# Kernel tuning notes

Measured on AMD Instinct MI355X. Metric: run time of the kernel, lower is better.

The kernel has to match this reference:

```python
import jax, jax.numpy as jnp
import numpy as np

V, E, HID, NLAYERS, NL, B, T = 21128, 512, 512, 2, 9, 64, 512
H = HID // 2  # per-direction hidden


def setup_inputs() -> dict:
    key = jax.random.key(0)
    ks = jax.random.split(key, 12)
    n = lambda k, sh, sc=0.05: (jax.random.normal(k, sh, dtype=jnp.float32) * sc)
    return {
        "input_ids": jax.random.randint(ks[0], (B, T), 0, V),
        "labels": jax.random.randint(ks[1], (B, T), 0, NL),
        "emb": n(ks[2], (V, E), 0.02),
        # stacked LSTM params: [layer, direction, ...]; layer0 input = E == HID
        "w_ih": n(ks[3], (NLAYERS, 2, 4 * H, HID)),
        "w_hh": n(ks[4], (NLAYERS, 2, 4 * H, H)),
        "b_ih": n(ks[5], (NLAYERS, 2, 4 * H)),
        "b_hh": n(ks[6], (NLAYERS, 2, 4 * H)),
        "cls_w": n(ks[7], (NL, HID)),
        "cls_b": n(ks[8], (NL,)),
        "start_trans": jax.random.uniform(ks[9], (NL,), jnp.float32, -0.1, 0.1),
        "end_trans": jax.random.uniform(ks[10], (NL,), jnp.float32, -0.1, 0.1),
        "trans": jax.random.uniform(ks[11], (NL, NL), jnp.float32, -0.1, 0.1),
    }


def _lstm_dir(x, wi, wh, bi, bh, reverse):
    # x: [B,T,I] -> h: [B,T,H]; torch gate order i,f,g,o
    xp = jnp.einsum('bti,gi->btg', x, wi) + bi + bh  # [B,T,4H]
    if reverse:
        xp = xp[:, ::-1]
    h0 = jnp.zeros((x.shape[0], wh.shape[1]), x.dtype)

    def step(carry, xt):
        h, c = carry
        g = xt + h @ wh.T
        i, f, gg, o = jnp.split(g, 4, axis=-1)
        c = jax.nn.sigmoid(f) * c + jax.nn.sigmoid(i) * jnp.tanh(gg)
        h = jax.nn.sigmoid(o) * jnp.tanh(c)
        return (h, c), h

    _, hs = jax.lax.scan(step, (h0, h0), xp.swapaxes(0, 1))
    hs = hs.swapaxes(0, 1)
    return hs[:, ::-1] if reverse else hs


def _crf_neg_llh(logits, labels, start_trans, end_trans, trans):
    # torchcrf forward, full mask, reduction='sum'; returns -sum(log-likelihood)
    em0 = logits[:, 0]  # [B,NL]
    alpha0 = start_trans[None, :] + em0
    num0 = start_trans[labels[:, 0]] + jnp.take_along_axis(em0, labels[:, 0:1], 1)[:, 0]

    def step(carry, xt):
        alpha, num, prev = carry
        em, tag = xt  # [B,NL], [B]
        alpha = jax.nn.logsumexp(alpha[:, :, None] + trans[None] + em[:, None, :], axis=1)
        num = num + trans[prev, tag] + jnp.take_along_axis(em, tag[:, None], 1)[:, 0]
        return (alpha, num, tag), None

    xs = (logits[:, 1:].swapaxes(0, 1), labels[:, 1:].swapaxes(0, 1))
    (alpha, num, last), _ = jax.lax.scan(step, (alpha0, num0, labels[:, 0]), xs)
    denom = jax.nn.logsumexp(alpha + end_trans[None, :], axis=1)
    num = num + end_trans[last]
    return -jnp.sum(num - denom)


def reference(input_ids, labels, emb, w_ih, w_hh, b_ih, b_hh, cls_w, cls_b,
              start_trans, end_trans, trans):
    x = emb[input_ids]  # [B,T,E]
    for l in range(NLAYERS):
        fwd = _lstm_dir(x, w_ih[l, 0], w_hh[l, 0], b_ih[l, 0], b_hh[l, 0], False)
        bwd = _lstm_dir(x, w_ih[l, 1], w_hh[l, 1], b_ih[l, 1], b_hh[l, 1], True)
        x = jnp.concatenate([fwd, bwd], axis=-1)  # [B,T,HID]
    logits = jnp.einsum('bth,lh->btl', x, cls_w) + cls_b  # [B,T,NL]
    return _crf_neg_llh(logits, labels, start_trans, end_trans, trans)
```

## Files before the change

kernel.cpp:

```cpp
#include <hip/hip_runtime.h>

#define B_   64
#define T_   512
#define HID_ 512
#define H_   256
#define G4   1024
#define N2   2048
#define M_   (B_*T_)
#define NL_  9

typedef short short8 __attribute__((ext_vector_type(8)));
typedef float f32x4 __attribute__((ext_vector_type(4)));
typedef _Float16 f16x2 __attribute__((ext_vector_type(2)));

__device__ inline float bf2f(unsigned short u) {
  unsigned int x = ((unsigned int)u) << 16;
  return __builtin_bit_cast(float, x);
}
__device__ inline unsigned short f2bf(float f) {
  unsigned int u = __builtin_bit_cast(unsigned int, f);
  return (unsigned short)((u + 0x7fffu + ((u >> 16) & 1u)) >> 16);
}
__device__ inline unsigned short f2h(float f) {
  _Float16 h = (_Float16)f;
  return __builtin_bit_cast(unsigned short, h);
}
__device__ inline float fdot2(unsigned int w, unsigned int h, float acc) {
#if __has_builtin(__builtin_amdgcn_fdot2)
  return __builtin_amdgcn_fdot2(__builtin_bit_cast(f16x2, w),
                                __builtin_bit_cast(f16x2, h), acc, false);
#else
  f16x2 a = __builtin_bit_cast(f16x2, w), b = __builtin_bit_cast(f16x2, h);
  return acc + (float)a[0]*(float)b[0] + (float)a[1]*(float)b[1];
#endif
}
__device__ inline float sigm(float x)     { return 1.f / (1.f + __expf(-x)); }
__device__ inline float tanhfast(float x) { return 1.f - 2.f / (__expf(2.f*x) + 1.f); }

__device__ inline float xhalf_sum(float x) {
#if __has_builtin(__builtin_amdgcn_permlane32_swap)
  typedef unsigned int u32x2 __attribute__((ext_vector_type(2)));
  u32x2 r = __builtin_amdgcn_permlane32_swap(
      __builtin_bit_cast(unsigned int, x), __builtin_bit_cast(unsigned int, x),
      false, false);
  return x + __builtin_bit_cast(float, r[1]);
#else
  return x + __shfl_xor(x, 32, 64);
#endif
}

__device__ inline void gload16(const unsigned short* g, unsigned short* l) {
  __builtin_amdgcn_global_load_lds(
      (const __attribute__((address_space(1))) void*)g,
      (__attribute__((address_space(3))) void*)l, 16, 0, 0);
}

__global__ void k_cast_bf16x4(const float4* __restrict__ src, ushort4* __restrict__ dst, int n4) {
  int i = blockIdx.x*256 + threadIdx.x;
  if (i < n4) {
    float4 v = src[i];
    ushort4 o;
    o.x = f2bf(v.x); o.y = f2bf(v.y); o.z = f2bf(v.z); o.w = f2bf(v.w);
    dst[i] = o;
  }
}

__global__ void k_pack_whh(const float* __restrict__ whh, unsigned int* __restrict__ wr,
                           unsigned int* __restrict__ wl) {
  int idx = blockIdx.x*256 + threadIdx.x;
  int q   = idx & 3;
  int t   = (idx >> 2) & 511;
  int i4  = (idx >> 11) & 63;
  int ld  = idx >> 17;
  int lane = t & 63, wave = t >> 6;
  int u  = wave*32 + (lane & 31);
  int kh = lane >> 5;
  int g, k0;
  if (i4 < 48) { g = i4/12; int j = i4%12; k0 = kh*128 + 8*j + 2*q; }
  else         { int m = i4-48; g = m>>2; int jl = m&3; k0 = kh*128 + 96 + 8*jl + 2*q; }
  int c = g*256 + u;
  const float* src = whh + ((size_t)ld*1024 + c)*256 + k0;
  unsigned int pack = (unsigned int)f2h(src[0]) | ((unsigned int)f2h(src[1]) << 16);
  if (i4 < 48) wr[(((size_t)ld*48 + i4)*512 + t)*4 + q] = pack;
  else         wl[(((size_t)ld*16 + (i4-48))*512 + t)*4 + q] = pack;
}

__global__ void k_bias_sum(const float* __restrict__ bi, const float* __restrict__ bh,
                           float* __restrict__ bs) {
  int i = blockIdx.x*256 + threadIdx.x;
  if (i < 4096) {
    int l = i >> 11, r = i & 2047;
    int dd = r >> 10, nn = r & 1023, g = nn >> 8, u = nn & 255;
    bs[l*2048 + dd*1024 + u*4 + g] = bi[i] + bh[i];
  }
}

__global__ void k_cls_pad(const float* __restrict__ w, unsigned short* __restrict__ dst) {
  int i = blockIdx.x*256 + threadIdx.x;
  if (i < 16*512) {
    int n = i >> 9, k = i & 511;
    dst[i] = (n < NL_) ? f2bf(w[n*512 + k]) : (unsigned short)0;
  }
}

__global__ void k_embed(const int* __restrict__ ids, const float* __restrict__ emb,
                        unsigned short* __restrict__ x0) {
  int idx = blockIdx.x*256 + threadIdx.x;
  int m  = idx >> 7;
  int e4 = (idx & 127) << 2;
  int id = ids[m];
  float4 v = *(const float4*)(emb + (size_t)id*HID_ + e4);
  ushort4 o;
  o.x = f2bf(v.x); o.y = f2bf(v.y); o.z = f2bf(v.z); o.w = f2bf(v.w);
  *(ushort4*)(x0 + (size_t)m*HID_ + e4) = o;
}

__global__ __launch_bounds__(256) void k_gemm_inproj(const unsigned short* __restrict__ A,
    const unsigned short* __restrict__ Bt, const float* __restrict__ bias,
    unsigned short* __restrict__ C) {
  __shared__ unsigned short As[2][4096];
  __shared__ unsigned short Bs[2][4096];
  int tid  = threadIdx.x;
  int lane = tid & 63, w = tid >> 6;
  int wm = w >> 1, wn = w & 1;
  int d  = blockIdx.x >> 3;
  int u0 = (blockIdx.x & 7) * 32;
  int m0 = blockIdx.y * 128;

  int c0 = tid, c1 = 256 + tid;
  int ar0 = c0 & 127, ak0 = c0 >> 7;
  int ar1 = c1 & 127, ak1 = c1 >> 7;
  int br0 = d*1024 + (ar0 >> 5)*256 + u0 + (ar0 & 31);
  int br1 = d*1024 + (ar1 >> 5)*256 + u0 + (ar1 & 31);
  const unsigned short* gA0 = A  + (size_t)(m0 + ar0)*512 + ak0*8;
  const unsigned short* gA1 = A  + (size_t)(m0 + ar1)*512 + ak1*8;
  const unsigned short* gB0 = Bt + (size_t)br0*512 + ak0*8;
  const unsigned short* gB1 = Bt + (size_t)br1*512 + ak1*8;

  int r = lane & 15, kg = lane >> 4;

  f32x4 acc[4][4];
  #pragma unroll
  for (int mi = 0; mi < 4; mi++)
    #pragma unroll
    for (int ni = 0; ni < 4; ni++)
      acc[mi][ni] = (f32x4){0,0,0,0};

  gload16(gA0, As[0] + c0*8); gload16(gA1, As[0] + c1*8);
  gload16(gB0, Bs[0] + c0*8); gload16(gB1, Bs[0] + c1*8);
  gA0 += 32; gA1 += 32; gB0 += 32; gB1 += 32;
  __syncthreads();

  int cur = 0;
  #pragma unroll 1
  for (int kt = 0; kt < 16; kt++) {
    if (kt < 15) {
      unsigned short* nA = As[cur^1];
      unsigned short* nB = Bs[cur^1];
      gload16(gA0, nA + c0*8); gload16(gA1, nA + c1*8);
      gload16(gB0, nB + c0*8); gload16(gB1, nB + c1*8);
      gA0 += 32; gA1 += 32; gB0 += 32; gB1 += 32;
    }
    const short8* Af = (const short8*)As[cur] + (size_t)kg*128 + wm*64 + r;
    const short8* Bf = (const short8*)Bs[cur] + (size_t)kg*128 + wn*16 + r;
    short8 av[4], bv[4];
    #pragma unroll
    for (int i = 0; i < 4; i++) { av[i] = Af[i*16]; bv[i] = Bf[i*32]; }
    #pragma unroll
    for (int mi = 0; mi < 4; mi++)
      #pragma unroll
      for (int ni = 0; ni < 4; ni++)
        acc[mi][ni] = __builtin_amdgcn_mfma_f32_16x16x32_bf16(av[mi], bv[ni], acc[mi][ni], 0, 0, 0);
    __syncthreads();
    cur ^= 1;
  }

  int rbase = m0 + wm*64 + (lane >> 4)*4;
  int ucol  = u0 + wn*16 + (lane & 15);
  float4 bb = *(const float4*)(bias + (size_t)d*1024 + ucol*4);
  #pragma unroll
  for (int mi = 0; mi < 4; mi++)
    #pragma unroll
    for (int rr = 0; rr < 4; rr++) {
      ushort4 o;
      o.x = f2bf(acc[mi][0][rr] + bb.x);
      o.y = f2bf(acc[mi][1][rr] + bb.y);
      o.z = f2bf(acc[mi][2][rr] + bb.z);
      o.w = f2bf(acc[mi][3][rr] + bb.w);
      *(ushort4*)(C + (size_t)(rbase + mi*16 + rr)*N2 + d*1024 + ucol*4) = o;
    }
}

__global__ __launch_bounds__(256) void k_cls(const unsigned short* __restrict__ X,
    const unsigned short* __restrict__ Wb, const float* __restrict__ cb,
    float* __restrict__ out) {
  int lane = threadIdx.x & 63, wave = threadIdx.x >> 6;
  int m0 = blockIdx.x*64 + wave*16;
  int r = lane & 15, kg = lane >> 4;
  const short8* Ap = (const short8*)(X  + (size_t)(m0 + r)*512 + kg*8);
  const short8* Bp = (const short8*)(Wb + (size_t)r*512 + kg*8);
  f32x4 acc = {0,0,0,0};
  #pragma unroll
  for (int kb = 0; kb < 16; kb++)
    acc = __builtin_amdgcn_mfma_f32_16x16x32_bf16(Ap[kb*4], Bp[kb*4], acc, 0, 0, 0);
  int row0 = m0 + (lane >> 4)*4, col = lane & 15;
  if (col < NL_) {
    float bb = cb[col];
    #pragma unroll
    for (int rr = 0; rr < 4; rr++)
      out[(size_t)(row0+rr)*NL_ + col] = acc[rr] + bb;
  }
}

#define DOT4(ACC, W0, W1, W2, W3, HH) do { \
  ACC = fdot2(W0, (HH).x, ACC); ACC = fdot2(W1, (HH).y, ACC); \
  ACC = fdot2(W2, (HH).z, ACC); ACC = fdot2(W3, (HH).w, ACC); } while(0)

__global__ __launch_bounds__(512, 2) void k_rec(const unsigned short* __restrict__ xp,
    const uint4* __restrict__ wr, const uint4* __restrict__ wl,
    unsigned short* __restrict__ xout, int layer) {
  extern __shared__ char smem[];
  unsigned int* hA = (unsigned int*)(smem + 131072);
  unsigned int* hB = hA + 128;
  int t = threadIdx.x;
  int lane = t & 63, wave = t >> 6;
  int u  = wave*32 + (lane & 31);
  int kh = lane >> 5;
  bool lo = (lane < 32);
  int b = blockIdx.x >> 1, d = blockIdx.x & 1;
  int ld = layer*2 + d;

  char* wlb = smem + (((unsigned)(t*16)) ^ (((unsigned)t & 0x38u) << 1));
  {
    const uint4* src = wl + (size_t)ld*16*512 + t;
    #pragma unroll
    for (int m = 0; m < 16; m++)
      *(uint4*)(wlb + m*8192) = src[(size_t)m*512];
  }
  uint4 wq[48];
  {
    const uint4* src = wr + (size_t)ld*48*512 + t;
    #pragma unroll
    for (int i = 0; i < 48; i++) wq[i] = src[(size_t)i*512];
  }
  if (t < 128) hA[t] = 0u;
  float cst = 0.f;
  const unsigned short* xbase = xp + (size_t)b*T_*N2 + (size_t)d*G4 + u*4;
  unsigned short* obase = xout + (size_t)b*T_*HID_ + d*H_ + u;
  __syncthreads();

  int tt = d ? (T_-1) : 0;
  ushort4 nx = *(const ushort4*)(xbase + (size_t)tt*N2);
  #pragma unroll 1
  for (int step = 0; step < T_; step++) {
    int ttn = d ? (T_-2-step) : (step+1);
    int ttc = (step < T_-1) ? ttn : tt;
    ushort4 cx = nx;
    nx = *(const ushort4*)(xbase + (size_t)ttc*N2);
    const uint4* hs = (const uint4*)((step & 1) ? hB : hA) + kh*16;
    float a0 = lo ? bf2f(cx.x) : 0.f;
    float a1 = lo ? bf2f(cx.y) : 0.f;
    float a2 = lo ? bf2f(cx.z) : 0.f;
    float a3 = lo ? bf2f(cx.w) : 0.f;
    #pragma unroll
    for (int j = 0; j < 12; j++) {
      uint4 hh = hs[j];
      DOT4(a0, wq[j].x,    wq[j].y,    wq[j].z,    wq[j].w,    hh);
      DOT4(a1, wq[12+j].x, wq[12+j].y, wq[12+j].z, wq[12+j].w, hh);
      DOT4(a2, wq[24+j].x, wq[24+j].y, wq[24+j].z, wq[24+j].w, hh);
      DOT4(a3, wq[36+j].x, wq[36+j].y, wq[36+j].z, wq[36+j].w, hh);
    }
    #pragma unroll
    for (int jl = 0; jl < 4; jl++) {
      uint4 hh = hs[12 + jl];
      uint4 q0 = *(const uint4*)(wlb + (0*4+jl)*8192);
      uint4 q1 = *(const uint4*)(wlb + (1*4+jl)*8192);
      uint4 q2 = *(const uint4*)(wlb + (2*4+jl)*8192);
      uint4 q3 = *(const uint4*)(wlb + (3*4+jl)*8192);
      DOT4(a0, q0.x, q0.y, q0.z, q0.w, hh);
      DOT4(a1, q1.x, q1.y, q1.z, q1.w, hh);
      DOT4(a2, q2.x, q2.y, q2.z, q2.w, hh);
      DOT4(a3, q3.x, q3.y, q3.z, q3.w, hh);
    }
    a0 = xhalf_sum(a0); a1 = xhalf_sum(a1);
    a2 = xhalf_sum(a2); a3 = xhalf_sum(a3);
    if (lo) {
      float gi = sigm(a0);
      float gf = sigm(a1);
      float gg = tanhfast(a2);
      float go = sigm(a3);
      cst = gf*cst + gi*gg;
      float h = go * tanhfast(cst);
      _Float16* hn = (_Float16*)((step & 1) ? hA : hB);
      hn[u] = (_Float16)h;
      obase[(size_t)tt*HID_] = f2bf(h);
    }
    asm volatile("s_waitcnt lgkmcnt(0)" ::: "memory");
    __builtin_amdgcn_s_barrier();
    tt = ttn;
  }
}

__global__ void k_zero(float* out) { if (threadIdx.x == 0) out[0] = 0.f; }

__global__ void k_crf(const float* __restrict__ logits, const int* __restrict__ labels,
                      const float* __restrict__ st, const float* __restrict__ et,
                      const float* __restrict__ tr, float* __restrict__ out) {
  int b = blockIdx.x, lane = threadIdx.x;
  bool act = lane < NL_;
  const float* lb = logits + (size_t)b*T_*NL_;
  float trc[9];
  #pragma unroll
  for (int i = 0; i < 9; i++) trc[i] = act ? tr[i*9 + lane] : 0.f;
  float em = act ? lb[lane] : -1e30f;
  float alpha = act ? (st[lane] + em) : -1e30f;
  int prev = labels[b*T_];
  float num = __shfl(alpha, prev);
  for (int ttt = 1; ttt < T_; ttt++) {
    em = act ? lb[ttt*NL_ + lane] : -1e30f;
    float vv[9]; float mx = -1e30f;
    #pragma unroll
    for (int i = 0; i < 9; i++) { vv[i] = __shfl(alpha, i) + trc[i]; mx = fmaxf(mx, vv[i]); }
    float s = 0.f;
    #pragma unroll
    for (int i = 0; i < 9; i++) s += __expf(vv[i] - mx);
    alpha = act ? (mx + __logf(s) + em) : -1e30f;
    int tag = labels[b*T_ + ttt];
    float emtag = __shfl(em, tag);
    if (lane == 0) num += tr[prev*9 + tag] + emtag;
    prev = tag;
  }
  float fa = act ? (alpha + et[lane]) : -1e30f;
  float mx = -1e30f;
  #pragma unroll
  for (int i = 0; i < 9; i++) mx = fmaxf(mx, __shfl(fa, i));
  float s = 0.f;
  #pragma unroll
  for (int i = 0; i < 9; i++) s += __expf(__shfl(fa, i) - mx);
  float denom = mx + __logf(s);
  if (lane == 0) {
    num += et[prev];
    atomicAdd(out, denom - num);
  }
}

extern "C" void kernel_launch(void* const* d_in, const int* in_sizes, int n_in,
                              void* d_out, int out_size, void* d_ws, size_t ws_size,
                              hipStream_t stream) {
  const int*   ids    = (const int*)d_in[0];
  const int*   labels = (const int*)d_in[1];
  const float* emb    = (const float*)d_in[2];
  const float* w_ih   = (const float*)d_in[3];
  const float* w_hh   = (const float*)d_in[4];
  const float* b_ih   = (const float*)d_in[5];
  const float* b_hh   = (const float*)d_in[6];
  const float* cls_w  = (const float*)d_in[7];
  const float* cls_b  = (const float*)d_in[8];
  const float* st     = (const float*)d_in[9];
  const float* et     = (const float*)d_in[10];
  const float* tr     = (const float*)d_in[11];
  float* out = (float*)d_out;

  char* ws = (char*)d_ws;
  unsigned short* xp    = (unsigned short*)(ws);
  unsigned short* x0    = (unsigned short*)(ws + 134217728);
  unsigned short* x1    = (unsigned short*)(ws + 167772160);
  unsigned short* wbi   = (unsigned short*)(ws + 201326592);
  unsigned int*   wreg  = (unsigned int*)  (ws + 205520896);
  unsigned int*   wldsg = (unsigned int*)  (ws + 207093760);
  float*          bsum  = (float*)         (ws + 207618048);
  unsigned short* clswb = (unsigned short*)(ws + 207634432);
  float*          logit = (float*)         (ws + 207650816);

  const int REC_SMEM = 131072 + 1024;
  hipFuncSetAttribute((const void*)k_rec, hipFuncAttributeMaxDynamicSharedMemorySize, REC_SMEM);

  k_cast_bf16x4<<<2048, 256, 0, stream>>>((const float4*)w_ih, (ushort4*)wbi, 2*N2*512/4);
  k_pack_whh <<<2048, 256, 0, stream>>>(w_hh, wreg, wldsg);
  k_bias_sum <<<16,   256, 0, stream>>>(b_ih, b_hh, bsum);
  k_cls_pad  <<<32,   256, 0, stream>>>(cls_w, clswb);
  k_embed    <<<16384,256, 0, stream>>>(ids, emb, x0);

  dim3 ggrid(16, 256);
  k_gemm_inproj<<<ggrid, 256, 0, stream>>>(x0, wbi, bsum, xp);
  k_rec<<<128, 512, REC_SMEM, stream>>>(xp, (const uint4*)wreg, (const uint4*)wldsg, x1, 0);
  k_gemm_inproj<<<ggrid, 256, 0, stream>>>(x1, wbi + (size_t)N2*512, bsum + 2048, xp);
  k_rec<<<128, 512, REC_SMEM, stream>>>(xp, (const uint4*)wreg, (const uint4*)wldsg, x0, 1);
  k_cls<<<512, 256, 0, stream>>>(x0, clswb, cls_b, logit);
  k_zero<<<1, 64, 0, stream>>>(out);
  k_crf<<<64, 64, 0, stream>>>(logit, labels, st, et, tr, out);
}
```

Before: 2.358 ms.

## Split recurrent hidden reduction four ways with two units per lane group

The recurrent LSTM kernel now splits the 256-wide hidden dot product into four 64-element quarters across lane groups of 16, and each lane group handles two hidden units (eight gate accumulators) instead of one unit split into halves. The weight packing is reorganized to match, the h buffer is padded per quarter to avoid LDS bank conflicts, and partial sums are combined with permlane32 and permlane16 swaps. The goal is more useful work per lane, so the gate nonlinearities run on a quarter of the lanes instead of half and the cross-lane reduction is shared. In exchange there is an extra reduction stage per gate and more accumulator registers.

New measurement: 2.925 ms. 24.0% more time.

```diff
diff --git a/kernel.cpp b/kernel.cpp
--- a/kernel.cpp
+++ b/kernel.cpp
@@ -12,6 +12,7 @@
 typedef short short8 __attribute__((ext_vector_type(8)));
 typedef float f32x4 __attribute__((ext_vector_type(4)));
 typedef _Float16 f16x2 __attribute__((ext_vector_type(2)));
+typedef unsigned int u32x2 __attribute__((ext_vector_type(2)));
 
 __device__ inline float bf2f(unsigned short u) {
   unsigned int x = ((unsigned int)u) << 16;
@@ -37,16 +38,24 @@
 __device__ inline float sigm(float x)     { return 1.f / (1.f + __expf(-x)); }
 __device__ inline float tanhfast(float x) { return 1.f - 2.f / (__expf(2.f*x) + 1.f); }
 
-__device__ inline float xhalf_sum(float x) {
+__device__ inline float qsum(float x) {
 #if __has_builtin(__builtin_amdgcn_permlane32_swap)
-  typedef unsigned int u32x2 __attribute__((ext_vector_type(2)));
   u32x2 r = __builtin_amdgcn_permlane32_swap(
       __builtin_bit_cast(unsigned int, x), __builtin_bit_cast(unsigned int, x),
       false, false);
-  return x + __builtin_bit_cast(float, r[1]);
+  x += __builtin_bit_cast(float, r[1]);
 #else
-  return x + __shfl_xor(x, 32, 64);
+  x += __shfl_xor(x, 32, 64);
 #endif
+#if __has_builtin(__builtin_amdgcn_permlane16_swap)
+  u32x2 s = __builtin_amdgcn_permlane16_swap(
+      __builtin_bit_cast(unsigned int, x), __builtin_bit_cast(unsigned int, x),
+      false, false);
+  x += __builtin_bit_cast(float, s[1]);
+#else
+  x += __shfl_xor(x, 16, 64);
+#endif
+  return x;
 }
 
 __device__ inline void gload16(const unsigned short* g, unsigned short* l) {
@@ -68,21 +77,23 @@
 __global__ void k_pack_whh(const float* __restrict__ whh, unsigned int* __restrict__ wr,
                            unsigned int* __restrict__ wl) {
   int idx = blockIdx.x*256 + threadIdx.x;
-  int q   = idx & 3;
+  int qq  = idx & 3;
   int t   = (idx >> 2) & 511;
   int i4  = (idx >> 11) & 63;
   int ld  = idx >> 17;
   int lane = t & 63, wave = t >> 6;
-  int u  = wave*32 + (lane & 31);
-  int kh = lane >> 5;
-  int g, k0;
-  if (i4 < 48) { g = i4/12; int j = i4%12; k0 = kh*128 + 8*j + 2*q; }
-  else         { int m = i4-48; g = m>>2; int jl = m&3; k0 = kh*128 + 96 + 8*jl + 2*q; }
-  int c = g*256 + u;
-  const float* src = whh + ((size_t)ld*1024 + c)*256 + k0;
+  int q = lane >> 4, p = lane & 15;
+  int P = wave*16 + p;
+  int c, j;
+  if (i4 < 48) { c = i4/6; j = i4%6; }
+  else         { int m = i4-48; c = m>>1; j = 6 + (m&1); }
+  int unit_sel = c >> 2, g = c & 3;
+  int col = g*256 + 2*P + unit_sel;
+  int k0  = q*64 + 8*j + 2*qq;
+  const float* src = whh + ((size_t)ld*1024 + col)*256 + k0;
   unsigned int pack = (unsigned int)f2h(src[0]) | ((unsigned int)f2h(src[1]) << 16);
-  if (i4 < 48) wr[(((size_t)ld*48 + i4)*512 + t)*4 + q] = pack;
-  else         wl[(((size_t)ld*16 + (i4-48))*512 + t)*4 + q] = pack;
+  if (i4 < 48) wr[(((size_t)ld*48 + i4)*512 + t)*4 + qq] = pack;
+  else         wl[(((size_t)ld*16 + (i4-48))*512 + t)*4 + qq] = pack;
 }
 
 __global__ void k_bias_sum(const float* __restrict__ bi, const float* __restrict__ bh,
@@ -220,13 +231,12 @@
     const uint4* __restrict__ wr, const uint4* __restrict__ wl,
     unsigned short* __restrict__ xout, int layer) {
   extern __shared__ char smem[];
-  unsigned int* hA = (unsigned int*)(smem + 131072);
-  unsigned int* hB = hA + 128;
+  char* hAb = smem + 131072;
+  char* hBb = hAb + 576;
   int t = threadIdx.x;
   int lane = t & 63, wave = t >> 6;
-  int u  = wave*32 + (lane & 31);
-  int kh = lane >> 5;
-  bool lo = (lane < 32);
+  int q = lane >> 4, p = lane & 15;
+  int P = wave*16 + p;
   int b = blockIdx.x >> 1, d = blockIdx.x & 1;
   int ld = layer*2 + d;
 
@@ -243,57 +253,76 @@
     #pragma unroll
     for (int i = 0; i < 48; i++) wq[i] = src[(size_t)i*512];
   }
-  if (t < 128) hA[t] = 0u;
-  float cst = 0.f;
-  const unsigned short* xbase = xp + (size_t)b*T_*N2 + (size_t)d*G4 + u*4;
-  unsigned short* obase = xout + (size_t)b*T_*HID_ + d*H_ + u;
+  if (t < 144) ((unsigned int*)hAb)[t] = 0u;
+  float cst0 = 0.f, cst1 = 0.f;
+  const unsigned short* xbase = xp + (size_t)b*T_*N2 + (size_t)d*G4 + P*8;
+  unsigned short* obase = xout + (size_t)b*T_*HID_ + d*H_ + 2*P;
+  int hwoff = ((2*P) >> 6)*144 + ((2*P) & 63)*2;
   __syncthreads();
 
   int tt = d ? (T_-1) : 0;
-  ushort4 nx = *(const ushort4*)(xbase + (size_t)tt*N2);
+  uint4 nx = *(const uint4*)(xbase + (size_t)tt*N2);
   #pragma unroll 1
   for (int step = 0; step < T_; step++) {
     int ttn = d ? (T_-2-step) : (step+1);
     int ttc = (step < T_-1) ? ttn : tt;
-    ushort4 cx = nx;
-    nx = *(const ushort4*)(xbase + (size_t)ttc*N2);
-    const uint4* hs = (const uint4*)((step & 1) ? hB : hA) + kh*16;
-    float a0 = lo ? bf2f(cx.x) : 0.f;
-    float a1 = lo ? bf2f(cx.y) : 0.f;
-    float a2 = lo ? bf2f(cx.z) : 0.f;
-    float a3 = lo ? bf2f(cx.w) : 0.f;
-    #pragma unroll
-    for (int j = 0; j < 12; j++) {
-      uint4 hh = hs[j];
+    uint4 cx = nx;
+    nx = *(const uint4*)(xbase + (size_t)ttc*N2);
+    const char* hb = ((step & 1) ? hBb : hAb) + q*144;
+    float a0=0.f,a1=0.f,a2=0.f,a3=0.f,a4=0.f,a5=0.f,a6=0.f,a7=0.f;
+    #pragma unroll
+    for (int j = 0; j < 6; j++) {
+      uint4 hh = *(const uint4*)(hb + j*16);
       DOT4(a0, wq[j].x,    wq[j].y,    wq[j].z,    wq[j].w,    hh);
-      DOT4(a1, wq[12+j].x, wq[12+j].y, wq[12+j].z, wq[12+j].w, hh);
-      DOT4(a2, wq[24+j].x, wq[24+j].y, wq[24+j].z, wq[24+j].w, hh);
-      DOT4(a3, wq[36+j].x, wq[36+j].y, wq[36+j].z, wq[36+j].w, hh);
+      DOT4(a1, wq[6+j].x,  wq[6+j].y,  wq[6+j].z,  wq[6+j].w,  hh);
+      DOT4(a2, wq[12+j].x, wq[12+j].y, wq[12+j].z, wq[12+j].w, hh);
+      DOT4(a3, wq[18+j].x, wq[18+j].y, wq[18+j].z, wq[18+j].w, hh);
+      DOT4(a4, wq[24+j].x, wq[24+j].y, wq[24+j].z, wq[24+j].w, hh);
+      DOT4(a5, wq[30+j].x, wq[30+j].y, wq[30+j].z, wq[30+j].w, hh);
+      DOT4(a6, wq[36+j].x, wq[36+j].y, wq[36+j].z, wq[36+j].w, hh);
+      DOT4(a7, wq[42+j].x, wq[42+j].y, wq[42+j].z, wq[42+j].w, hh);
     }
     #pragma unroll
-    for (int jl = 0; jl < 4; jl++) {
-      uint4 hh = hs[12 + jl];
-      uint4 q0 = *(const uint4*)(wlb + (0*4+jl)*8192);
-      uint4 q1 = *(const uint4*)(wlb + (1*4+jl)*8192);
-      uint4 q2 = *(const uint4*)(wlb + (2*4+jl)*8192);
-      uint4 q3 = *(const uint4*)(wlb + (3*4+jl)*8192);
+    for (int jj = 0; jj < 2; jj++) {
+      uint4 hh = *(const uint4*)(hb + (6+jj)*16);
+      uint4 q0 = *(const uint4*)(wlb + (0*2+jj)*8192);
+      uint4 q1 = *(const uint4*)(wlb + (1*2+jj)*8192);
+      uint4 q2 = *(const uint4*)(wlb + (2*2+jj)*8192);
+      uint4 q3 = *(const uint4*)(wlb + (3*2+jj)*8192);
+      uint4 q4 = *(const uint4*)(wlb + (4*2+jj)*8192);
+      uint4 q5 = *(const uint4*)(wlb + (5*2+jj)*8192);
+      uint4 q6 = *(const uint4*)(wlb + (6*2+jj)*8192);
+      uint4 q7 = *(const uint4*)(wlb + (7*2+jj)*8192);
       DOT4(a0, q0.x, q0.y, q0.z, q0.w, hh);
       DOT4(a1, q1.x, q1.y, q1.z, q1.w, hh);
       DOT4(a2, q2.x, q2.y, q2.z, q2.w, hh);
       DOT4(a3, q3.x, q3.y, q3.z, q3.w, hh);
+      DOT4(a4, q4.x, q4.y, q4.z, q4.w, hh);
+      DOT4(a5, q5.x, q5.y, q5.z, q5.w, hh);
+      DOT4(a6, q6.x, q6.y, q6.z, q6.w, hh);
+      DOT4(a7, q7.x, q7.y, q7.z, q7.w, hh);
     }
-    a0 = xhalf_sum(a0); a1 = xhalf_sum(a1);
-    a2 = xhalf_sum(a2); a3 = xhalf_sum(a3);
-    if (lo) {
-      float gi = sigm(a0);
-      float gf = sigm(a1);
-      float gg = tanhfast(a2);
-      float go = sigm(a3);
-      cst = gf*cst + gi*gg;
-      float h = go * tanhfast(cst);
-      _Float16* hn = (_Float16*)((step & 1) ? hA : hB);
-      hn[u] = (_Float16)h;
-      obase[(size_t)tt*HID_] = f2bf(h);
+    a0 = qsum(a0); a1 = qsum(a1); a2 = qsum(a2); a3 = qsum(a3);
+    a4 = qsum(a4); a5 = qsum(a5); a6 = qsum(a6); a7 = qsum(a7);
+    if (q == 0) {
+      float gi0 = sigm(a0 + bf2f((unsigned short)(cx.x & 0xffff)));
+      float gf0 = sigm(a1 + bf2f((unsigned short)(cx.x >> 16)));
+      float gg0 = tanhfast(a2 + bf2f((unsigned short)(cx.y & 0xffff)));
+      float go0 = sigm(a3 + bf2f((unsigned short)(cx.y >> 16)));
+      cst0 = gf0*cst0 + gi0*gg0;
+      float h0 = go0 * tanhfast(cst0);
+      float gi1 = sigm(a4 + bf2f((unsigned short)(cx.z & 0xffff)));
+      float gf1 = sigm(a5 + bf2f((unsigned short)(cx.z >> 16)));
+      float gg1 = tanhfast(a6 + bf2f((unsigned short)(cx.w & 0xffff)));
+      float go1 = sigm(a7 + bf2f((unsigned short)(cx.w >> 16)));
+      cst1 = gf1*cst1 + gi1*gg1;
+      float h1 = go1 * tanhfast(cst1);
+      char* hn = (step & 1) ? hAb : hBb;
+      unsigned int hp = (unsigned int)__builtin_bit_cast(unsigned short, (_Float16)h0)
+                      | ((unsigned int)__builtin_bit_cast(unsigned short, (_Float16)h1) << 16);
+      *(unsigned int*)(hn + hwoff) = hp;
+      unsigned int ob = (unsigned int)f2bf(h0) | ((unsigned int)f2bf(h1) << 16);
+      *(unsigned int*)(obase + (size_t)tt*HID_) = ob;
     }
     asm volatile("s_waitcnt lgkmcnt(0)" ::: "memory");
     __builtin_amdgcn_s_barrier();
@@ -372,7 +401,7 @@
   unsigned short* clswb = (unsigned short*)(ws + 207634432);
   float*          logit = (float*)         (ws + 207650816);
 
-  const int REC_SMEM = 131072 + 1024;
+  const int REC_SMEM = 131072 + 1280;
   hipFuncSetAttribute((const void*)k_rec, hipFuncAttributeMaxDynamicSharedMemorySize, REC_SMEM);
 
   k_cast_bf16x4<<<2048, 256, 0, stream>>>((const float4*)w_ih, (ushort4*)wbi, 2*N2*512/4);
```
